# Kernel optimization log

Measured on AMD Instinct MI355X. Metric: run time of the kernel, lower is better.

Reference implementation:

```python
import jax, jax.numpy as jnp
import numpy as np

N = 100000      # nodes
E = 1600000     # edges (avg degree 16)
NF = 1          # node_feature_dim
EF = 1          # edge_feature_dim
H = 64          # hidden_dim
L = 5           # num_layers


def _linear_init(key, fan_in, fan_out):
    # torch nn.Linear default: U(-1/sqrt(fan_in), 1/sqrt(fan_in)) for W and b
    s = 1.0 / np.sqrt(fan_in)
    kw, kb = jax.random.split(key)
    w = jax.random.uniform(kw, (fan_in, fan_out), minval=-s, maxval=s, dtype=jnp.float32)
    b = jax.random.uniform(kb, (fan_out,), minval=-s, maxval=s, dtype=jnp.float32)
    return w, b


def setup_inputs() -> dict:
    key = jax.random.key(0)
    ks = jax.random.split(key, 8)
    x = jax.random.normal(ks[0], (N, NF), dtype=jnp.float32)
    edge_index = jax.random.randint(ks[1], (2, E), 0, N, dtype=jnp.int32)
    edge_attr = jax.random.uniform(ks[2], (E, EF), dtype=jnp.float32)

    emb_w, emb_b = _linear_init(ks[3], NF, H)
    fc_w, fc_b = _linear_init(ks[4], H, 1)

    msg_w1, msg_b1, msg_w2, msg_b2 = [], [], [], []
    upd_w1, upd_b1, upd_w2, upd_b2 = [], [], [], []
    lk = jax.random.split(ks[5], L)
    for l in range(L):
        k1, k2, k3, k4 = jax.random.split(lk[l], 4)
        w, b = _linear_init(k1, H + EF, H); msg_w1.append(w); msg_b1.append(b)
        w, b = _linear_init(k2, H, H);      msg_w2.append(w); msg_b2.append(b)
        w, b = _linear_init(k3, 2 * H, H);  upd_w1.append(w); upd_b1.append(b)
        w, b = _linear_init(k4, H, H);      upd_w2.append(w); upd_b2.append(b)

    stack = lambda xs: jnp.stack(xs, axis=0)
    return {
        "x": x, "edge_index": edge_index, "edge_attr": edge_attr,
        "emb_w": emb_w, "emb_b": emb_b,
        "msg_w1": stack(msg_w1), "msg_b1": stack(msg_b1),
        "msg_w2": stack(msg_w2), "msg_b2": stack(msg_b2),
        "upd_w1": stack(upd_w1), "upd_b1": stack(upd_b1),
        "upd_w2": stack(upd_w2), "upd_b2": stack(upd_b2),
        "fc_w": fc_w, "fc_b": fc_b,
    }


def reference(x, edge_index, edge_attr, emb_w, emb_b,
              msg_w1, msg_b1, msg_w2, msg_b2,
              upd_w1, upd_b1, upd_w2, upd_b2, fc_w, fc_b):
    src = edge_index[0]  # x_j (source)
    dst = edge_index[1]  # aggregation target i
    n = x.shape[0]

    h = x @ emb_w + emb_b  # [N, H]
    for l in range(msg_w1.shape[0]):
        # message: MLP(cat[x_j, edge_attr])
        m = jnp.concatenate([h[src], edge_attr], axis=1)  # [E, H+EF]
        m = jax.nn.relu(m @ msg_w1[l] + msg_b1[l]) @ msg_w2[l] + msg_b2[l]  # [E, H]
        # scatter-min aggregate; torch_scatter fills empty segments with 0
        aggr = jax.ops.segment_min(m, dst, num_segments=n)
        aggr = jnp.where(jnp.isfinite(aggr), aggr, jnp.zeros_like(aggr))
        # update: MLP(cat[x, aggr])
        u = jnp.concatenate([h, aggr], axis=1)  # [N, 2H]
        h = jax.nn.relu(u @ upd_w1[l] + upd_b1[l]) @ upd_w2[l] + upd_b2[l]
    return (h @ fc_w + fc_b).squeeze(-1)  # [N]
```

## Files before the change

kernel.cpp:

```cpp
#include <hip/hip_runtime.h>
#include <math.h>

#define N_NODES 100000
#define N_EDGES 1600000
#define HDIM 64
#define SCAN_T 1024
#define SCAN_CHUNK 98
#define NPB 64
#define LBLOCKS 1563
#define BSTR 36

__device__ __forceinline__ unsigned encMin(float f) {
  unsigned u = __float_as_uint(f);
  return (u & 0x80000000u) ? ~u : (u | 0x80000000u);
}
__device__ __forceinline__ float decMin(unsigned u) {
  unsigned b = (u & 0x80000000u) ? (u & 0x7FFFFFFFu) : ~u;
  return __uint_as_float(b);
}


__global__ __launch_bounds__(256) void k_zero_int(int* __restrict__ p, int n) {
  int i = blockIdx.x * 256 + threadIdx.x;
  if (i < n) p[i] = 0;
}

__global__ __launch_bounds__(256) void k_deg_count(const int* __restrict__ ei,
                                                   int* __restrict__ deg) {
  int e = blockIdx.x * 256 + threadIdx.x;
  if (e < N_EDGES) atomicAdd(&deg[ei[N_EDGES + e]], 1);
}

__global__ __launch_bounds__(SCAN_T) void k_rowptr(const int* __restrict__ deg,
                                                   int* __restrict__ row_ptr) {
  __shared__ int sums[SCAN_T];
  const int t = threadIdx.x;
  const int lo = t * SCAN_CHUNK;
  const int hi = min(lo + SCAN_CHUNK, N_NODES);
  int s = 0;
  for (int i = lo; i < hi; ++i) s += deg[i];
  sums[t] = s;
  __syncthreads();
  for (int off = 1; off < SCAN_T; off <<= 1) {
    int v = (t >= off) ? sums[t - off] : 0;
    __syncthreads();
    sums[t] += v;
    __syncthreads();
  }
  int run = (t == 0) ? 0 : sums[t - 1];
  for (int i = lo; i < hi; ++i) { row_ptr[i] = run; run += deg[i]; }
  if (t == SCAN_T - 1) row_ptr[N_NODES] = run;
}

__global__ __launch_bounds__(256) void k_scatter(
    const int* __restrict__ ei, const float* __restrict__ eattr,
    const int* __restrict__ row_ptr, int* __restrict__ cursor,
    int* __restrict__ s_sd, float* __restrict__ s_ea) {
  int e = blockIdx.x * 256 + threadIdx.x;
  if (e >= N_EDGES) return;
  int d = ei[N_EDGES + e];
  int pos = row_ptr[d] + atomicAdd(&cursor[d], 1);
  s_sd[pos] = ei[e] | ((d & (NPB - 1)) << 20);
  s_ea[pos] = eattr[e];
}


__global__ __launch_bounds__(256) void k_embed_z(
    const float* __restrict__ x, const float* __restrict__ emb_w,
    const float* __restrict__ emb_b,
    const float* __restrict__ w1, const float* __restrict__ b1,
    float* __restrict__ h, float* __restrict__ z) {
  __shared__ float hs[64][65];
  const int t = threadIdx.x;
  const int nl = t >> 2;
  const int l4 = t & 3;
  const int i = blockIdx.x * 64 + nl;
  const bool valid = (i < N_NODES);
  const int jbase = l4 * 16;
  const float xv = valid ? x[i] : 0.0f;

  float hv[16];
  #pragma unroll
  for (int jj = 0; jj < 16; ++jj) {
    int j = jbase + jj;
    hv[jj] = fmaf(xv, emb_w[j], emb_b[j]);
    hs[nl][j] = hv[jj];
  }
  if (valid) {
    #pragma unroll
    for (int q = 0; q < 4; ++q)
      reinterpret_cast<float4*>(h + (size_t)i * HDIM)[l4 * 4 + q] =
          make_float4(hv[4*q], hv[4*q+1], hv[4*q+2], hv[4*q+3]);
  }
  __syncthreads();

  float acc[16];
  #pragma unroll
  for (int jj = 0; jj < 16; ++jj) acc[jj] = b1[jbase + jj];
  #pragma unroll 8
  for (int k = 0; k < 64; ++k) {
    float hk = hs[nl][k];
    const float* wr = w1 + k * 64 + jbase;
    #pragma unroll
    for (int jj = 0; jj < 16; ++jj) acc[jj] = fmaf(hk, wr[jj], acc[jj]);
  }
  if (valid) {
    #pragma unroll
    for (int q = 0; q < 4; ++q)
      reinterpret_cast<float4*>(z + (size_t)i * HDIM)[l4 * 4 + q] =
          make_float4(acc[4*q], acc[4*q+1], acc[4*q+2], acc[4*q+3]);
  }
}

template <int LAST>
__global__ __launch_bounds__(256) void k_layer(
    const int* __restrict__ row_ptr,
    const int* __restrict__ s_sd, const float* __restrict__ s_ea,
    const float* __restrict__ z_in,
    const float* __restrict__ w1b, const float* __restrict__ w2,
    const float* __restrict__ b2,
    const float* __restrict__ u1w, const float* __restrict__ u1b,
    const float* __restrict__ u2w, const float* __restrict__ u2b,
    const float* __restrict__ w1next, const float* __restrict__ b1next,
    const float* __restrict__ fcw, const float* __restrict__ fcb,
    float* __restrict__ h, float* __restrict__ z_out, float* __restrict__ out) {
  __shared__ float buf[4][64][BSTR];
  __shared__ unsigned acc_u[NPB][65];
  __shared__ float ps[NPB][4];
  float* acc_f = (float*)acc_u;

  const int t = threadIdx.x;
  const int lane = t & 63;
  const int wv = __builtin_amdgcn_readfirstlane(t >> 6);
  const int nbase = blockIdx.x * NPB;

  for (int i = t; i < NPB * 65; i += 256) ((unsigned*)acc_u)[i] = 0xFFFFFFFFu;

  const int eb0 = row_ptr[nbase];
  const int eb1 = row_ptr[min(nbase + NPB, N_NODES)];
  const int n = eb1 - eb0;
  const int we0 = eb0 + (n * wv) / 4;
  const int we1 = eb0 + (n * (wv + 1)) / 4;
  const int rq = lane >> 3;
  const int q  = lane & 7;
  float* mybuf = &buf[wv][0][0];
  __syncthreads();

  for (int base = we0; base < we1; base += 64) {
    const int cnt = min(64, we1 - base);

    float m[64];
    #pragma unroll
    for (int c = 0; c < 64; ++c) m[c] = b2[c];

    #pragma unroll
    for (int half = 0; half < 2; ++half) {
      const float4 w1bq = ((const float4*)w1b)[half * 8 + q];
      #pragma unroll
      for (int r = 0; r < 8; ++r) {
        const int row = r * 8 + rq;
        if (row < cnt) {
          const int sd = s_sd[base + row];
          const float ea = s_ea[base + row];
          const int src = sd & 0xFFFFF;
          float4 zq = ((const float4*)(z_in + (size_t)src * HDIM))[half * 8 + q];
          float4 hv;
          hv.x = fmaxf(fmaf(ea, w1bq.x, zq.x), 0.f);
          hv.y = fmaxf(fmaf(ea, w1bq.y, zq.y), 0.f);
          hv.z = fmaxf(fmaf(ea, w1bq.z, zq.z), 0.f);
          hv.w = fmaxf(fmaf(ea, w1bq.w, zq.w), 0.f);
          *(float4*)&mybuf[row * BSTR + q * 4] = hv;
        }
      }
      const float* bp = &mybuf[lane * BSTR];
      #pragma unroll 4
      for (int k2 = 0; k2 < 16; ++k2) {
        float2 hq = *(const float2*)&bp[k2 * 2];
        const float* wr0 = w2 + (half * 32 + 2 * k2) * 64;
        const float* wr1 = wr0 + 64;
        #pragma unroll
        for (int c = 0; c < 64; ++c) m[c] = fmaf(hq.x, wr0[c], m[c]);
        #pragma unroll
        for (int c = 0; c < 64; ++c) m[c] = fmaf(hq.y, wr1[c], m[c]);
      }
    }
    if (lane < cnt) {
      const int dl = s_sd[base + lane] >> 20;
      #pragma unroll
      for (int c = 0; c < 64; ++c)
        atomicMin(&acc_u[dl][c], encMin(m[c]));
    }
  }
  __syncthreads();

  const int jq = wv * 16;
  const int node = nbase + lane;
  const bool valid = (node < N_NODES);
  const size_t off = (size_t)(valid ? node : 0) * HDIM;

  #pragma unroll
  for (int j = 0; j < 16; ++j) {
    float f = decMin(acc_u[lane][jq + j]);
    if (!isfinite(f)) f = 0.f;
    acc_f[lane * 65 + jq + j] = f;
  }
  __syncthreads();

  float acc[16];
  #pragma unroll
  for (int j = 0; j < 16; ++j) acc[j] = u1b[jq + j];
  {
    const float4* hr = reinterpret_cast<const float4*>(h + off);
    for (int k4 = 0; k4 < 16; ++k4) {
      float4 uv = hr[k4];
      const float* w0 = u1w + (4*k4+0) * 64 + jq;
      const float* w1r = u1w + (4*k4+1) * 64 + jq;
      const float* w2r = u1w + (4*k4+2) * 64 + jq;
      const float* w3 = u1w + (4*k4+3) * 64 + jq;
      #pragma unroll
      for (int j = 0; j < 16; ++j) acc[j] = fmaf(uv.x, w0[j], acc[j]);
      #pragma unroll
      for (int j = 0; j < 16; ++j) acc[j] = fmaf(uv.y, w1r[j], acc[j]);
      #pragma unroll
      for (int j = 0; j < 16; ++j) acc[j] = fmaf(uv.z, w2r[j], acc[j]);
      #pragma unroll
      for (int j = 0; j < 16; ++j) acc[j] = fmaf(uv.w, w3[j], acc[j]);
    }
    #pragma unroll 4
    for (int k = 0; k < 64; ++k) {
      float uk = acc_f[lane * 65 + k];
      const float* wr = u1w + (64 + k) * 64 + jq;
      #pragma unroll
      for (int j = 0; j < 16; ++j) acc[j] = fmaf(uk, wr[j], acc[j]);
    }
  }
  __syncthreads();
  #pragma unroll
  for (int j = 0; j < 16; ++j) acc_f[lane * 65 + jq + j] = fmaxf(acc[j], 0.f);
  __syncthreads();

  float hn[16];
  #pragma unroll
  for (int j = 0; j < 16; ++j) hn[j] = u2b[jq + j];
  #pragma unroll 4
  for (int k = 0; k < 64; ++k) {
    float hk = acc_f[lane * 65 + k];
    const float* wr = u2w + k * 64 + jq;
    #pragma unroll
    for (int j = 0; j < 16; ++j) hn[j] = fmaf(hk, wr[j], hn[j]);
  }
  if (valid) {
    #pragma unroll
    for (int v4 = 0; v4 < 4; ++v4)
      reinterpret_cast<float4*>(h + off)[wv * 4 + v4] =
          make_float4(hn[4*v4], hn[4*v4+1], hn[4*v4+2], hn[4*v4+3]);
  }

  if (LAST) {
    float s = 0.0f;
    #pragma unroll
    for (int j = 0; j < 16; ++j) s = fmaf(hn[j], fcw[jq + j], s);
    ps[lane][wv] = s;
    __syncthreads();
    if (wv == 0 && valid)
      out[node] = ps[lane][0] + ps[lane][1] + ps[lane][2] + ps[lane][3] + fcb[0];
  } else {
    __syncthreads();
    #pragma unroll
    for (int j = 0; j < 16; ++j) acc_f[lane * 65 + jq + j] = hn[j];
    __syncthreads();
    float zz[16];
    #pragma unroll
    for (int j = 0; j < 16; ++j) zz[j] = b1next[jq + j];
    #pragma unroll 4
    for (int k = 0; k < 64; ++k) {
      float hk = acc_f[lane * 65 + k];
      const float* wr = w1next + k * 64 + jq;
      #pragma unroll
      for (int j = 0; j < 16; ++j) zz[j] = fmaf(hk, wr[j], zz[j]);
    }
    if (valid) {
      #pragma unroll
      for (int v4 = 0; v4 < 4; ++v4)
        reinterpret_cast<float4*>(z_out + off)[wv * 4 + v4] =
            make_float4(zz[4*v4], zz[4*v4+1], zz[4*v4+2], zz[4*v4+3]);
    }
  }
}

extern "C" void kernel_launch(void* const* d_in, const int* in_sizes, int n_in,
                              void* d_out, int out_size, void* d_ws, size_t ws_size,
                              hipStream_t stream) {
  const float* x      = (const float*)d_in[0];
  const int*   ei     = (const int*)d_in[1];
  const float* eattr  = (const float*)d_in[2];
  const float* emb_w  = (const float*)d_in[3];
  const float* emb_b  = (const float*)d_in[4];
  const float* msg_w1 = (const float*)d_in[5];
  const float* msg_b1 = (const float*)d_in[6];
  const float* msg_w2 = (const float*)d_in[7];
  const float* msg_b2 = (const float*)d_in[8];
  const float* upd_w1 = (const float*)d_in[9];
  const float* upd_b1 = (const float*)d_in[10];
  const float* upd_w2 = (const float*)d_in[11];
  const float* upd_b2 = (const float*)d_in[12];
  const float* fc_w   = (const float*)d_in[13];
  const float* fc_b   = (const float*)d_in[14];
  float* out = (float*)d_out;

  float* h     = (float*)d_ws;
  float* zA    = h + (size_t)N_NODES * HDIM;
  float* zB    = zA + (size_t)N_NODES * HDIM;
  float* s_ea  = zB + (size_t)N_NODES * HDIM;
  int*   s_sd  = (int*)(s_ea + N_EDGES);
  int*   row_ptr = s_sd + N_EDGES;
  int*   deg   = row_ptr + (N_NODES + 1);
  int*   cursor= deg + N_NODES;

  const int nodeBlocks64 = (N_NODES + 63) / 64;
  const int edgeBlocks = (N_EDGES + 255) / 256;

  k_zero_int<<<(2 * N_NODES + 255) / 256, 256, 0, stream>>>(deg, 2 * N_NODES);
  k_deg_count<<<edgeBlocks, 256, 0, stream>>>(ei, deg);
  k_rowptr<<<1, SCAN_T, 0, stream>>>(deg, row_ptr);
  k_scatter<<<edgeBlocks, 256, 0, stream>>>(ei, eattr, row_ptr, cursor, s_sd, s_ea);

  k_embed_z<<<nodeBlocks64, 256, 0, stream>>>(x, emb_w, emb_b, msg_w1, msg_b1, h, zA);

  float* zin = zA;
  float* zout = zB;
  for (int l = 0; l < 5; ++l) {
    const float* w1b = msg_w1 + l * 65 * 64 + 64 * 64;
    const float* w2  = msg_w2 + l * 64 * 64;
    const float* b2  = msg_b2 + l * 64;
    const float* u1w = upd_w1 + l * 128 * 64;
    const float* u1b = upd_b1 + l * 64;
    const float* u2w = upd_w2 + l * 64 * 64;
    const float* u2b = upd_b2 + l * 64;
    if (l < 4) {
      k_layer<0><<<LBLOCKS, 256, 0, stream>>>(
          row_ptr, s_sd, s_ea, zin,
          w1b, w2, b2, u1w, u1b, u2w, u2b,
          msg_w1 + (l + 1) * 65 * 64, msg_b1 + (l + 1) * 64,
          nullptr, nullptr,
          h, zout, nullptr);
      float* tmp = zin; zin = zout; zout = tmp;
    } else {
      k_layer<1><<<LBLOCKS, 256, 0, stream>>>(
          row_ptr, s_sd, s_ea, zin,
          w1b, w2, b2, u1w, u1b, u2w, u2b,
          nullptr, nullptr,
          fc_w, fc_b,
          h, nullptr, out);
    }
  }
}
```

Measured before the change: 2.732 ms.

## Segment-reduce edge messages in LDS before shared-memory atomicMin

Instead of each lane issuing 64 LDS atomicMin ops for its own edge, the wave writes messages to its LDS buffer in two 32-column halves, transposes the layout, and walks edges sorted by destination. It keeps a running min and issues one atomic per destination run. The buffer stride changes from 36 to 34 with float2 stores to reduce bank conflicts. This relies on edges within a wave being grouped by destination, and it adds a serial loop of shuffles and LDS reads.

```diff
diff --git a/kernel.cpp b/kernel.cpp
--- a/kernel.cpp
+++ b/kernel.cpp
@@ -8,7 +8,7 @@
 #define SCAN_CHUNK 98
 #define NPB 64
 #define LBLOCKS 1563
-#define BSTR 36
+#define BSTR 34
 
 __device__ __forceinline__ unsigned encMin(float f) {
   unsigned u = __float_as_uint(f);
@@ -143,11 +143,15 @@
   const int we1 = eb0 + (n * (wv + 1)) / 4;
   const int rq = lane >> 3;
   const int q  = lane & 7;
+  const int eg = lane >> 5;
+  const int cl = lane & 31;
   float* mybuf = &buf[wv][0][0];
   __syncthreads();
 
   for (int base = we0; base < we1; base += 64) {
     const int cnt = min(64, we1 - base);
+    const int sdv = (lane < cnt) ? s_sd[base + lane] : 0;
+    const int dlv = sdv >> 20;
 
     float m[64];
     #pragma unroll
@@ -164,12 +168,13 @@
           const float ea = s_ea[base + row];
           const int src = sd & 0xFFFFF;
           float4 zq = ((const float4*)(z_in + (size_t)src * HDIM))[half * 8 + q];
-          float4 hv;
-          hv.x = fmaxf(fmaf(ea, w1bq.x, zq.x), 0.f);
-          hv.y = fmaxf(fmaf(ea, w1bq.y, zq.y), 0.f);
-          hv.z = fmaxf(fmaf(ea, w1bq.z, zq.z), 0.f);
-          hv.w = fmaxf(fmaf(ea, w1bq.w, zq.w), 0.f);
-          *(float4*)&mybuf[row * BSTR + q * 4] = hv;
+          float2 h0, h1;
+          h0.x = fmaxf(fmaf(ea, w1bq.x, zq.x), 0.f);
+          h0.y = fmaxf(fmaf(ea, w1bq.y, zq.y), 0.f);
+          h1.x = fmaxf(fmaf(ea, w1bq.z, zq.z), 0.f);
+          h1.y = fmaxf(fmaf(ea, w1bq.w, zq.w), 0.f);
+          *(float2*)&mybuf[row * BSTR + q * 4]     = h0;
+          *(float2*)&mybuf[row * BSTR + q * 4 + 2] = h1;
         }
       }
       const float* bp = &mybuf[lane * BSTR];
@@ -184,11 +189,31 @@
         for (int c = 0; c < 64; ++c) m[c] = fmaf(hq.y, wr1[c], m[c]);
       }
     }
-    if (lane < cnt) {
-      const int dl = s_sd[base + lane] >> 20;
-      #pragma unroll
-      for (int c = 0; c < 64; ++c)
-        atomicMin(&acc_u[dl][c], encMin(m[c]));
+
+    #pragma unroll
+    for (int ch = 0; ch < 2; ++ch) {
+      asm volatile("s_waitcnt lgkmcnt(0)" ::: "memory");
+      if (lane < cnt) {
+        #pragma unroll
+        for (int j2 = 0; j2 < 16; ++j2)
+          *(float2*)&mybuf[lane * BSTR + 2 * j2] =
+              make_float2(m[ch * 32 + 2 * j2], m[ch * 32 + 2 * j2 + 1]);
+      }
+      asm volatile("s_waitcnt lgkmcnt(0)" ::: "memory");
+      float run = INFINITY;
+      int cur = -1;
+      for (int i = 0; i < 32; ++i) {
+        const int e = eg * 32 + i;
+        if (e >= cnt) break;
+        const int dl = __shfl(dlv, e);
+        const float v = mybuf[e * BSTR + cl];
+        if (dl != cur) {
+          if (cur >= 0) atomicMin(&acc_u[cur][ch * 32 + cl], encMin(run));
+          cur = dl; run = INFINITY;
+        }
+        run = fminf(run, v);
+      }
+      if (cur >= 0) atomicMin(&acc_u[cur][ch * 32 + cl], encMin(run));
     }
   }
   __syncthreads();
```

After: 2.543 ms. 6.9% less time.
